# Optimization experiments

Measured on AMD Instinct MI355X. Metric: run time of the kernel, lower is better.

Reference implementation:

```python
import jax, jax.numpy as jnp
import numpy as np

N = 8192
D = 512
EPS = 1e-12  # F.normalize default eps


def setup_inputs() -> dict:
    key = jax.random.key(0)
    k1, k2 = jax.random.split(key)
    cur = jax.random.normal(k1, (N, D), dtype=jnp.float32)
    # randn -> mixed-sign entries, so every row of (incidence_m > 0) is unique
    # (the only case where the original `incidence_m += head` shapes agree).
    incidence_m = jax.random.normal(k2, (N, N), dtype=jnp.float32)
    return {"cur": cur, "incidence_m": incidence_m}


def reference(cur, incidence_m):
    # construct_directed: dedup rows of (incidence_m > 0); with all rows unique,
    # each node is its own hyperedge leader and head == mask as float, row order
    # preserved. head is built from python ints in torch, hence non-differentiable.
    mask = incidence_m > 0
    head = jax.lax.stop_gradient(mask.astype(incidence_m.dtype))  # [N, N]
    # F.normalize(head, dim=-1): L2 per row with eps clamp
    head = head / jnp.maximum(
        jnp.sqrt(jnp.sum(head * head, axis=-1, keepdims=True)), EPS
    )
    inc = incidence_m + head                          # [N, N]
    edge_fea = inc @ cur                              # [N, D]
    edge_degree = jnp.sum(inc, axis=-1, keepdims=True)  # [N, 1]
    return edge_fea / edge_degree
```

## Files before the change

### kernel.cpp

```cpp
#include <hip/hip_runtime.h>
#include <stdint.h>


#define NROWS 8192
#define DDIM  512

typedef float f32x4 __attribute__((ext_vector_type(4)));
typedef short s16x8 __attribute__((ext_vector_type(8)));

__device__ __forceinline__ unsigned short f2bf(float f) {
  union { float f; unsigned int u; } c; c.f = f;
  unsigned int u = c.u;
  unsigned int r = u + 0x7FFFu + ((u >> 16) & 1u);
  return (unsigned short)(r >> 16);
}

__global__ __launch_bounds__(256) void bprep_kernel(const float* __restrict__ cur,
                                                    unsigned char* __restrict__ bws) {
  int idx = blockIdx.x * 256 + threadIdx.x;
  int n = idx & 511;
  int kg9 = idx >> 9;
  int kt = kg9 >> 3;
  int kg = kg9 & 7;
  int k0 = kt * 64 + kg * 8;
  union { unsigned short h[8]; uint4 q; } u;
#pragma unroll
  for (int e = 0; e < 8; ++e)
    u.h[e] = f2bf(cur[(size_t)(k0 + e) * DDIM + n]);
  int nt = n >> 8, nn = n & 255;
  size_t off = ((size_t)(nt * 128 + kt) << 15) + ((size_t)kg << 12) + ((size_t)nn << 4);
  *(uint4*)(bws + off) = u.q;
}


#define FENCE() __builtin_amdgcn_sched_barrier(0)
#define BARRIER() __builtin_amdgcn_s_barrier()
#define WAITLGKM() asm volatile("s_waitcnt lgkmcnt(0)" ::: "memory")
#define MFMA_ __builtin_amdgcn_mfma_f32_16x16x32_bf16

__global__ __launch_bounds__(512, 4) void gemm_kernel(const float* __restrict__ inc,
                                                      const unsigned char* __restrict__ bws,
                                                      float* __restrict__ out) {
  __shared__ __align__(16) unsigned char smem[16512];
  unsigned char* const buf0 = smem;
  unsigned char* const buf1 = smem + 8192;

  const int tid = threadIdx.x;
  const int lane = tid & 63;
  const int wv = tid >> 6;
  const int r = lane & 15;
  const int q = lane >> 4;

  const int id = blockIdx.x;
  const int nt = (id & 7) >> 2;
  const int mt = (id >> 3) * 4 + (id & 3);
  const int brow = mt * 32;

  const int sm = tid >> 4;
  const int sp = tid & 15;
  const int kgw = sp >> 1, half = sp & 1;
  const float4* gAr = (const float4*)(inc + (size_t)(brow + sm) * NROWS) + sp;
  const int aWr = (kgw << 9) + ((sm ^ kgw) << 4) + (half << 3);

  int aOff[2][2];
#pragma unroll
  for (int kh = 0; kh < 2; ++kh)
#pragma unroll
    for (int rg = 0; rg < 2; ++rg) {
      int kg = kh * 4 + q;
      int row = rg * 16 + r;
      aOff[kh][rg] = (kg << 9) + ((row ^ kg) << 4);
    }

  const unsigned char* gB = bws + ((size_t)(nt * 128) << 15);
  int bOff[4];
#pragma unroll
  for (int kh = 0; kh < 2; ++kh)
#pragma unroll
    for (int cg = 0; cg < 2; ++cg)
      bOff[kh * 2 + cg] = ((kh * 4 + q) << 12) + ((wv * 32 + cg * 16 + r) << 4);

  f32x4 acc1[2][2], acc2[2][2];
#pragma unroll
  for (int a = 0; a < 2; ++a)
#pragma unroll
    for (int b = 0; b < 2; ++b) {
      acc1[a][b] = (f32x4){0.f, 0.f, 0.f, 0.f};
      acc2[a][b] = (f32x4){0.f, 0.f, 0.f, 0.f};
    }

  double s1 = 0.0;
  int cnt = 0;
  float4 x, y;
  s16x8 bX[4], bY[4];

#define ISSUE_A(d, KT) do { d = gAr[(KT) * 16]; } while (0)

#define LOADB(BS, KT) do {                                                                \
    const unsigned char* _g = gB + ((size_t)(KT) << 15);                                  \
    BS[0] = *(const s16x8*)(_g + bOff[0]);                                                \
    BS[1] = *(const s16x8*)(_g + bOff[1]);                                                \
    BS[2] = *(const s16x8*)(_g + bOff[2]);                                                \
    BS[3] = *(const s16x8*)(_g + bOff[3]);                                                \
  } while (0)

#define XFORM(v, BUF) do {                                                                \
    s1 += (double)v.x + (double)v.y + (double)v.z + (double)v.w;                          \
    cnt += (v.x > 0.f) + (v.y > 0.f) + (v.z > 0.f) + (v.w > 0.f);                         \
    unsigned dlo, dhi;                                                                    \
    asm("v_cvt_pk_bf16_f32 %0, %1, %2" : "=v"(dlo) : "v"(v.x), "v"(v.y));                 \
    asm("v_cvt_pk_bf16_f32 %0, %1, %2" : "=v"(dhi) : "v"(v.z), "v"(v.w));                 \
    unsigned mlo = (v.x > 0.f ? 0x3F80u : 0u) | (v.y > 0.f ? 0x3F800000u : 0u);           \
    unsigned mhi = (v.z > 0.f ? 0x3F80u : 0u) | (v.w > 0.f ? 0x3F800000u : 0u);           \
    *(unsigned long long*)((BUF) + aWr) =                                                 \
        (unsigned long long)dlo | ((unsigned long long)dhi << 32);                        \
    *(unsigned long long*)((BUF) + 4096 + aWr) =                                          \
        (unsigned long long)mlo | ((unsigned long long)mhi << 32);                        \
  } while (0)

#define MFMA_TILE(BUF, BS) do {                                                           \
    _Pragma("unroll")                                                                     \
    for (int kh = 0; kh < 2; ++kh) {                                                      \
      s16x8 af0 = *(const s16x8*)((BUF) + aOff[kh][0]);                                   \
      s16x8 af1 = *(const s16x8*)((BUF) + aOff[kh][1]);                                   \
      s16x8 mf0 = *(const s16x8*)((BUF) + 4096 + aOff[kh][0]);                            \
      s16x8 mf1 = *(const s16x8*)((BUF) + 4096 + aOff[kh][1]);                            \
      __builtin_amdgcn_s_setprio(1);                                                      \
      acc1[0][0] = MFMA_(af0, BS[kh * 2 + 0], acc1[0][0], 0, 0, 0);                       \
      acc2[0][0] = MFMA_(mf0, BS[kh * 2 + 0], acc2[0][0], 0, 0, 0);                       \
      acc1[0][1] = MFMA_(af0, BS[kh * 2 + 1], acc1[0][1], 0, 0, 0);                       \
      acc2[0][1] = MFMA_(mf0, BS[kh * 2 + 1], acc2[0][1], 0, 0, 0);                       \
      acc1[1][0] = MFMA_(af1, BS[kh * 2 + 0], acc1[1][0], 0, 0, 0);                       \
      acc2[1][0] = MFMA_(mf1, BS[kh * 2 + 0], acc2[1][0], 0, 0, 0);                       \
      acc1[1][1] = MFMA_(af1, BS[kh * 2 + 1], acc1[1][1], 0, 0, 0);                       \
      acc2[1][1] = MFMA_(mf1, BS[kh * 2 + 1], acc2[1][1], 0, 0, 0);                       \
      __builtin_amdgcn_s_setprio(0);                                                      \
    }                                                                                     \
  } while (0)

#define SYNC() do { FENCE(); WAITLGKM(); FENCE(); BARRIER(); FENCE(); } while (0)

  ISSUE_A(x, 0);
  LOADB(bX, 0);
  ISSUE_A(y, 1);
  XFORM(x, buf0);
  SYNC();

  for (int kt = 0; kt < 126; kt += 2) {
    ISSUE_A(x, kt + 2);
    LOADB(bY, kt + 1);
    FENCE();
    MFMA_TILE(buf0, bX);
    XFORM(y, buf1);
    SYNC();
    ISSUE_A(y, kt + 3);
    LOADB(bX, kt + 2);
    FENCE();
    MFMA_TILE(buf1, bY);
    XFORM(x, buf0);
    SYNC();
  }

  LOADB(bY, 127);
  FENCE();
  MFMA_TILE(buf0, bX);
  XFORM(y, buf1);
  SYNC();
  MFMA_TILE(buf1, bY);

#pragma unroll
  for (int o = 1; o < 16; o <<= 1) {
    s1 += __shfl_xor(s1, o);
    cnt += __shfl_xor(cnt, o);
  }
  __syncthreads();
  float* const invsS = (float*)buf0;
  float* const rdegS = invsS + 32;
  if (sp == 0) {
    double sq = sqrt((double)cnt);
    invsS[sm] = (cnt > 0) ? (float)(1.0 / sq) : 0.0f;
    rdegS[sm] = (float)(1.0 / (s1 + sq));
  }
  __syncthreads();

#pragma unroll
  for (int rg = 0; rg < 2; ++rg) {
#pragma unroll
    for (int cg = 0; cg < 2; ++cg) {
#pragma unroll
      for (int j = 0; j < 4; ++j) {
        int row = rg * 16 + q * 4 + j;
        out[(size_t)(brow + row) * DDIM + nt * 256 + wv * 32 + cg * 16 + r] =
            (acc1[rg][cg][j] + invsS[row] * acc2[rg][cg][j]) * rdegS[row];
      }
    }
  }
#undef ISSUE_A
#undef LOADB
#undef XFORM
#undef MFMA_TILE
#undef SYNC
}

extern "C" void kernel_launch(void* const* d_in, const int* in_sizes, int n_in,
                              void* d_out, int out_size, void* d_ws, size_t ws_size,
                              hipStream_t stream) {
  const float* cur = (const float*)d_in[0];
  const float* incm = (const float*)d_in[1];
  float* out = (float*)d_out;
  unsigned char* bws = (unsigned char*)d_ws;

  hipLaunchKernelGGL(bprep_kernel, dim3((NROWS * DDIM / 8) / 256), dim3(256), 0, stream,
                     cur, bws);
  hipLaunchKernelGGL(gemm_kernel, dim3(512), dim3(512), 0, stream, incm, bws, out);
}
```

Before: 166.9 us.

## Retile waves to 2x4 grid with half-tile B prefetch pipelining

```diff
diff --git a/kernel.cpp b/kernel.cpp
--- a/kernel.cpp
+++ b/kernel.cpp
@@ -48,6 +48,8 @@
   const int tid = threadIdx.x;
   const int lane = tid & 63;
   const int wv = tid >> 6;
+  const int wr = wv >> 2;
+  const int wc = wv & 3;
   const int r = lane & 15;
   const int q = lane >> 4;
 
@@ -62,46 +64,42 @@
   const float4* gAr = (const float4*)(inc + (size_t)(brow + sm) * NROWS) + sp;
   const int aWr = (kgw << 9) + ((sm ^ kgw) << 4) + (half << 3);
 
-  int aOff[2][2];
+  int aOff[2];
+#pragma unroll
+  for (int kh = 0; kh < 2; ++kh) {
+    int kg = kh * 4 + q;
+    int row = wr * 16 + r;
+    aOff[kh] = (kg << 9) + ((row ^ kg) << 4);
+  }
+
+  const unsigned char* gB = bws + ((size_t)(nt * 128) << 15);
+  int bOff[2][4];
 #pragma unroll
   for (int kh = 0; kh < 2; ++kh)
 #pragma unroll
-    for (int rg = 0; rg < 2; ++rg) {
-      int kg = kh * 4 + q;
-      int row = rg * 16 + r;
-      aOff[kh][rg] = (kg << 9) + ((row ^ kg) << 4);
-    }
-
-  const unsigned char* gB = bws + ((size_t)(nt * 128) << 15);
-  int bOff[4];
-#pragma unroll
-  for (int kh = 0; kh < 2; ++kh)
-#pragma unroll
-    for (int cg = 0; cg < 2; ++cg)
-      bOff[kh * 2 + cg] = ((kh * 4 + q) << 12) + ((wv * 32 + cg * 16 + r) << 4);
-
-  f32x4 acc1[2][2], acc2[2][2];
-#pragma unroll
-  for (int a = 0; a < 2; ++a)
-#pragma unroll
-    for (int b = 0; b < 2; ++b) {
-      acc1[a][b] = (f32x4){0.f, 0.f, 0.f, 0.f};
-      acc2[a][b] = (f32x4){0.f, 0.f, 0.f, 0.f};
-    }
+    for (int cg = 0; cg < 4; ++cg)
+      bOff[kh][cg] = ((kh * 4 + q) << 12) + ((wc * 64 + cg * 16 + r) << 4);
+
+  f32x4 acc1[4], acc2[4];
+#pragma unroll
+  for (int b = 0; b < 4; ++b) {
+    acc1[b] = (f32x4){0.f, 0.f, 0.f, 0.f};
+    acc2[b] = (f32x4){0.f, 0.f, 0.f, 0.f};
+  }
 
   double s1 = 0.0;
   int cnt = 0;
   float4 x, y;
-  s16x8 bX[4], bY[4];
+  s16x8 bA[4], bB[4];
 
 #define ISSUE_A(d, KT) do { d = gAr[(KT) * 16]; } while (0)
 
-#define LOADB(BS, KT) do {                                                                \
+#define LOADB(BS, KT, KH) do {                                                            \
     const unsigned char* _g = gB + ((size_t)(KT) << 15);                                  \
-    BS[0] = *(const s16x8*)(_g + bOff[0]);                                                \
-    BS[1] = *(const s16x8*)(_g + bOff[1]);                                                \
-    BS[2] = *(const s16x8*)(_g + bOff[2]);                                                \
-    BS[3] = *(const s16x8*)(_g + bOff[3]);                                                \
+    BS[0] = *(const s16x8*)(_g + bOff[KH][0]);                                            \
+    BS[1] = *(const s16x8*)(_g + bOff[KH][1]);                                            \
+    BS[2] = *(const s16x8*)(_g + bOff[KH][2]);                                            \
+    BS[3] = *(const s16x8*)(_g + bOff[KH][3]);                                            \
   } while (0)
 
 #define XFORM(v, BUF) do {                                                                \
@@ -118,55 +116,63 @@
         (unsigned long long)mlo | ((unsigned long long)mhi << 32);                        \
   } while (0)
 
-#define MFMA_TILE(BUF, BS) do {                                                           \
-    _Pragma("unroll")                                                                     \
-    for (int kh = 0; kh < 2; ++kh) {                                                      \
-      s16x8 af0 = *(const s16x8*)((BUF) + aOff[kh][0]);                                   \
-      s16x8 af1 = *(const s16x8*)((BUF) + aOff[kh][1]);                                   \
-      s16x8 mf0 = *(const s16x8*)((BUF) + 4096 + aOff[kh][0]);                            \
-      s16x8 mf1 = *(const s16x8*)((BUF) + 4096 + aOff[kh][1]);                            \
-      __builtin_amdgcn_s_setprio(1);                                                      \
-      acc1[0][0] = MFMA_(af0, BS[kh * 2 + 0], acc1[0][0], 0, 0, 0);                       \
-      acc2[0][0] = MFMA_(mf0, BS[kh * 2 + 0], acc2[0][0], 0, 0, 0);                       \
-      acc1[0][1] = MFMA_(af0, BS[kh * 2 + 1], acc1[0][1], 0, 0, 0);                       \
-      acc2[0][1] = MFMA_(mf0, BS[kh * 2 + 1], acc2[0][1], 0, 0, 0);                       \
-      acc1[1][0] = MFMA_(af1, BS[kh * 2 + 0], acc1[1][0], 0, 0, 0);                       \
-      acc2[1][0] = MFMA_(mf1, BS[kh * 2 + 0], acc2[1][0], 0, 0, 0);                       \
-      acc1[1][1] = MFMA_(af1, BS[kh * 2 + 1], acc1[1][1], 0, 0, 0);                       \
-      acc2[1][1] = MFMA_(mf1, BS[kh * 2 + 1], acc2[1][1], 0, 0, 0);                       \
-      __builtin_amdgcn_s_setprio(0);                                                      \
-    }                                                                                     \
+#define MFMA_KH(BUF, KH, BS) do {                                                         \
+    s16x8 af = *(const s16x8*)((BUF) + aOff[KH]);                                         \
+    s16x8 mf = *(const s16x8*)((BUF) + 4096 + aOff[KH]);                                  \
+    __builtin_amdgcn_s_setprio(1);                                                        \
+    acc1[0] = MFMA_(af, BS[0], acc1[0], 0, 0, 0);                                         \
+    acc2[0] = MFMA_(mf, BS[0], acc2[0], 0, 0, 0);                                         \
+    acc1[1] = MFMA_(af, BS[1], acc1[1], 0, 0, 0);                                         \
+    acc2[1] = MFMA_(mf, BS[1], acc2[1], 0, 0, 0);                                         \
+    acc1[2] = MFMA_(af, BS[2], acc1[2], 0, 0, 0);                                         \
+    acc2[2] = MFMA_(mf, BS[2], acc2[2], 0, 0, 0);                                         \
+    acc1[3] = MFMA_(af, BS[3], acc1[3], 0, 0, 0);                                         \
+    acc2[3] = MFMA_(mf, BS[3], acc2[3], 0, 0, 0);                                         \
+    __builtin_amdgcn_s_setprio(0);                                                        \
   } while (0)
 
 #define SYNC() do { FENCE(); WAITLGKM(); FENCE(); BARRIER(); FENCE(); } while (0)
 
   ISSUE_A(x, 0);
-  LOADB(bX, 0);
+  LOADB(bA, 0, 0);
   ISSUE_A(y, 1);
   XFORM(x, buf0);
   SYNC();
 
   for (int kt = 0; kt < 126; kt += 2) {
     ISSUE_A(x, kt + 2);
-    LOADB(bY, kt + 1);
-    FENCE();
-    MFMA_TILE(buf0, bX);
+    LOADB(bB, kt, 1);
+    FENCE();
+    MFMA_KH(buf0, 0, bA);
+    LOADB(bA, kt + 1, 0);
+    FENCE();
+    MFMA_KH(buf0, 1, bB);
     XFORM(y, buf1);
     SYNC();
     ISSUE_A(y, kt + 3);
-    LOADB(bX, kt + 2);
-    FENCE();
-    MFMA_TILE(buf1, bY);
+    LOADB(bB, kt + 1, 1);
+    FENCE();
+    MFMA_KH(buf1, 0, bA);
+    LOADB(bA, kt + 2, 0);
+    FENCE();
+    MFMA_KH(buf1, 1, bB);
     XFORM(x, buf0);
     SYNC();
   }
 
-  LOADB(bY, 127);
-  FENCE();
-  MFMA_TILE(buf0, bX);
+  LOADB(bB, 126, 1);
+  FENCE();
+  MFMA_KH(buf0, 0, bA);
+  LOADB(bA, 127, 0);
+  FENCE();
+  MFMA_KH(buf0, 1, bB);
   XFORM(y, buf1);
   SYNC();
-  MFMA_TILE(buf1, bY);
+  LOADB(bB, 127, 1);
+  FENCE();
+  MFMA_KH(buf1, 0, bA);
+  FENCE();
+  MFMA_KH(buf1, 1, bB);
 
 #pragma unroll
   for (int o = 1; o < 16; o <<= 1) {
@@ -184,21 +190,18 @@
   __syncthreads();
 
 #pragma unroll
-  for (int rg = 0; rg < 2; ++rg) {
-#pragma unroll
-    for (int cg = 0; cg < 2; ++cg) {
-#pragma unroll
-      for (int j = 0; j < 4; ++j) {
-        int row = rg * 16 + q * 4 + j;
-        out[(size_t)(brow + row) * DDIM + nt * 256 + wv * 32 + cg * 16 + r] =
-            (acc1[rg][cg][j] + invsS[row] * acc2[rg][cg][j]) * rdegS[row];
-      }
+  for (int cg = 0; cg < 4; ++cg) {
+#pragma unroll
+    for (int j = 0; j < 4; ++j) {
+      int row = wr * 16 + q * 4 + j;
+      out[(size_t)(brow + row) * DDIM + nt * 256 + wc * 64 + cg * 16 + r] =
+          (acc1[cg][j] + invsS[row] * acc2[cg][j]) * rdegS[row];
     }
   }
 #undef ISSUE_A
 #undef LOADB
 #undef XFORM
-#undef MFMA_TILE
+#undef MFMA_KH
 #undef SYNC
 }
 
```

New measurement: 232.3 us. 39.1% more time.

## Deepen A-tile pipeline to four LDS buffers with two barriers per four k-tiles

Applied to the files above, without the earlier changes.

```diff
diff --git a/kernel.cpp b/kernel.cpp
--- a/kernel.cpp
+++ b/kernel.cpp
@@ -41,9 +41,11 @@
 __global__ __launch_bounds__(512, 4) void gemm_kernel(const float* __restrict__ inc,
                                                       const unsigned char* __restrict__ bws,
                                                       float* __restrict__ out) {
-  __shared__ __align__(16) unsigned char smem[16512];
+  __shared__ __align__(16) unsigned char smem[32768];
   unsigned char* const buf0 = smem;
   unsigned char* const buf1 = smem + 8192;
+  unsigned char* const buf2 = smem + 16384;
+  unsigned char* const buf3 = smem + 24576;
 
   const int tid = threadIdx.x;
   const int lane = tid & 63;
@@ -91,7 +93,7 @@
 
   double s1 = 0.0;
   int cnt = 0;
-  float4 x, y;
+  float4 x0, y0, x1, y1;
   s16x8 bX[4], bY[4];
 
 #define ISSUE_A(d, KT) do { d = gAr[(KT) * 16]; } while (0)
@@ -140,33 +142,55 @@
 
 #define SYNC() do { FENCE(); WAITLGKM(); FENCE(); BARRIER(); FENCE(); } while (0)
 
-  ISSUE_A(x, 0);
+  ISSUE_A(x0, 0);
   LOADB(bX, 0);
-  ISSUE_A(y, 1);
-  XFORM(x, buf0);
+  ISSUE_A(y0, 1);
+  ISSUE_A(x1, 2);
+  ISSUE_A(y1, 3);
+  XFORM(x0, buf0);
+  XFORM(y0, buf1);
   SYNC();
 
-  for (int kt = 0; kt < 126; kt += 2) {
-    ISSUE_A(x, kt + 2);
-    LOADB(bY, kt + 1);
+  for (int i = 0; i < 31; ++i) {
+    const int t = i * 4;
+    ISSUE_A(x0, t + 4);
+    ISSUE_A(y0, t + 5);
+    LOADB(bY, t + 1);
     FENCE();
     MFMA_TILE(buf0, bX);
-    XFORM(y, buf1);
+    XFORM(x1, buf2);
+    LOADB(bX, t + 2);
+    FENCE();
+    MFMA_TILE(buf1, bY);
+    XFORM(y1, buf3);
     SYNC();
-    ISSUE_A(y, kt + 3);
-    LOADB(bX, kt + 2);
-    FENCE();
-    MFMA_TILE(buf1, bY);
-    XFORM(x, buf0);
+    ISSUE_A(x1, t + 6);
+    ISSUE_A(y1, t + 7);
+    LOADB(bY, t + 3);
+    FENCE();
+    MFMA_TILE(buf2, bX);
+    XFORM(x0, buf0);
+    LOADB(bX, t + 4);
+    FENCE();
+    MFMA_TILE(buf3, bY);
+    XFORM(y0, buf1);
     SYNC();
   }
 
+  LOADB(bY, 125);
+  FENCE();
+  MFMA_TILE(buf0, bX);
+  XFORM(x1, buf2);
+  LOADB(bX, 126);
+  FENCE();
+  MFMA_TILE(buf1, bY);
+  XFORM(y1, buf3);
+  SYNC();
   LOADB(bY, 127);
   FENCE();
-  MFMA_TILE(buf0, bX);
-  XFORM(y, buf1);
-  SYNC();
-  MFMA_TILE(buf1, bY);
+  MFMA_TILE(buf2, bX);
+  FENCE();
+  MFMA_TILE(buf3, bY);
 
 #pragma unroll
   for (int o = 1; o < 16; o <<= 1) {
```

New measurement: 176.1 us. 5.5% more time.

## Split waves into value and mask roles with wider column tiles, reduce via LDS

Applied to the files above, without the earlier changes.

```diff
diff --git a/kernel.cpp b/kernel.cpp
--- a/kernel.cpp
+++ b/kernel.cpp
@@ -41,13 +41,18 @@
 __global__ __launch_bounds__(512, 4) void gemm_kernel(const float* __restrict__ inc,
                                                       const unsigned char* __restrict__ bws,
                                                       float* __restrict__ out) {
-  __shared__ __align__(16) unsigned char smem[16512];
+  __shared__ __align__(16) unsigned char smem[33024];
   unsigned char* const buf0 = smem;
   unsigned char* const buf1 = smem + 8192;
+  float* const invsS = (float*)(smem + 32768);
+  float* const rdegS = invsS + 32;
 
   const int tid = threadIdx.x;
   const int lane = tid & 63;
   const int wv = tid >> 6;
+  const int wc = wv & 3;
+  const int role = wv >> 2;
+  const int roleOff = role << 12;
   const int r = lane & 15;
   const int q = lane >> 4;
 
@@ -73,26 +78,24 @@
     }
 
   const unsigned char* gB = bws + ((size_t)(nt * 128) << 15);
-  int bOff[4];
+  int bOff[8];
 #pragma unroll
   for (int kh = 0; kh < 2; ++kh)
 #pragma unroll
-    for (int cg = 0; cg < 2; ++cg)
-      bOff[kh * 2 + cg] = ((kh * 4 + q) << 12) + ((wv * 32 + cg * 16 + r) << 4);
-
-  f32x4 acc1[2][2], acc2[2][2];
+    for (int cg = 0; cg < 4; ++cg)
+      bOff[kh * 4 + cg] = ((kh * 4 + q) << 12) + ((wc * 64 + cg * 16 + r) << 4);
+
+  f32x4 acc[2][4];
 #pragma unroll
   for (int a = 0; a < 2; ++a)
 #pragma unroll
-    for (int b = 0; b < 2; ++b) {
-      acc1[a][b] = (f32x4){0.f, 0.f, 0.f, 0.f};
-      acc2[a][b] = (f32x4){0.f, 0.f, 0.f, 0.f};
-    }
+    for (int b = 0; b < 4; ++b)
+      acc[a][b] = (f32x4){0.f, 0.f, 0.f, 0.f};
 
   double s1 = 0.0;
   int cnt = 0;
   float4 x, y;
-  s16x8 bX[4], bY[4];
+  s16x8 bX[8], bY[8];
 
 #define ISSUE_A(d, KT) do { d = gAr[(KT) * 16]; } while (0)
 
@@ -102,6 +105,10 @@
     BS[1] = *(const s16x8*)(_g + bOff[1]);                                                \
     BS[2] = *(const s16x8*)(_g + bOff[2]);                                                \
     BS[3] = *(const s16x8*)(_g + bOff[3]);                                                \
+    BS[4] = *(const s16x8*)(_g + bOff[4]);                                                \
+    BS[5] = *(const s16x8*)(_g + bOff[5]);                                                \
+    BS[6] = *(const s16x8*)(_g + bOff[6]);                                                \
+    BS[7] = *(const s16x8*)(_g + bOff[7]);                                                \
   } while (0)
 
 #define XFORM(v, BUF) do {                                                                \
@@ -121,19 +128,17 @@
 #define MFMA_TILE(BUF, BS) do {                                                           \
     _Pragma("unroll")                                                                     \
     for (int kh = 0; kh < 2; ++kh) {                                                      \
-      s16x8 af0 = *(const s16x8*)((BUF) + aOff[kh][0]);                                   \
-      s16x8 af1 = *(const s16x8*)((BUF) + aOff[kh][1]);                                   \
-      s16x8 mf0 = *(const s16x8*)((BUF) + 4096 + aOff[kh][0]);                            \
-      s16x8 mf1 = *(const s16x8*)((BUF) + 4096 + aOff[kh][1]);                            \
+      s16x8 f0 = *(const s16x8*)((BUF) + roleOff + aOff[kh][0]);                          \
+      s16x8 f1 = *(const s16x8*)((BUF) + roleOff + aOff[kh][1]);                          \
       __builtin_amdgcn_s_setprio(1);                                                      \
-      acc1[0][0] = MFMA_(af0, BS[kh * 2 + 0], acc1[0][0], 0, 0, 0);                       \
-      acc2[0][0] = MFMA_(mf0, BS[kh * 2 + 0], acc2[0][0], 0, 0, 0);                       \
-      acc1[0][1] = MFMA_(af0, BS[kh * 2 + 1], acc1[0][1], 0, 0, 0);                       \
-      acc2[0][1] = MFMA_(mf0, BS[kh * 2 + 1], acc2[0][1], 0, 0, 0);                       \
-      acc1[1][0] = MFMA_(af1, BS[kh * 2 + 0], acc1[1][0], 0, 0, 0);                       \
-      acc2[1][0] = MFMA_(mf1, BS[kh * 2 + 0], acc2[1][0], 0, 0, 0);                       \
-      acc1[1][1] = MFMA_(af1, BS[kh * 2 + 1], acc1[1][1], 0, 0, 0);                       \
-      acc2[1][1] = MFMA_(mf1, BS[kh * 2 + 1], acc2[1][1], 0, 0, 0);                       \
+      acc[0][0] = MFMA_(f0, BS[kh * 4 + 0], acc[0][0], 0, 0, 0);                          \
+      acc[0][1] = MFMA_(f0, BS[kh * 4 + 1], acc[0][1], 0, 0, 0);                          \
+      acc[0][2] = MFMA_(f0, BS[kh * 4 + 2], acc[0][2], 0, 0, 0);                          \
+      acc[0][3] = MFMA_(f0, BS[kh * 4 + 3], acc[0][3], 0, 0, 0);                          \
+      acc[1][0] = MFMA_(f1, BS[kh * 4 + 0], acc[1][0], 0, 0, 0);                          \
+      acc[1][1] = MFMA_(f1, BS[kh * 4 + 1], acc[1][1], 0, 0, 0);                          \
+      acc[1][2] = MFMA_(f1, BS[kh * 4 + 2], acc[1][2], 0, 0, 0);                          \
+      acc[1][3] = MFMA_(f1, BS[kh * 4 + 3], acc[1][3], 0, 0, 0);                          \
       __builtin_amdgcn_s_setprio(0);                                                      \
     }                                                                                     \
   } while (0)
@@ -174,8 +179,6 @@
     cnt += __shfl_xor(cnt, o);
   }
   __syncthreads();
-  float* const invsS = (float*)buf0;
-  float* const rdegS = invsS + 32;
   if (sp == 0) {
     double sq = sqrt((double)cnt);
     invsS[sm] = (cnt > 0) ? (float)(1.0 / sq) : 0.0f;
@@ -183,17 +186,31 @@
   }
   __syncthreads();
 
-#pragma unroll
-  for (int rg = 0; rg < 2; ++rg) {
-#pragma unroll
-    for (int cg = 0; cg < 2; ++cg) {
-#pragma unroll
-      for (int j = 0; j < 4; ++j) {
-        int row = rg * 16 + q * 4 + j;
-        out[(size_t)(brow + row) * DDIM + nt * 256 + wv * 32 + cg * 16 + r] =
-            (acc1[rg][cg][j] + invsS[row] * acc2[rg][cg][j]) * rdegS[row];
-      }
-    }
+  float* const eBuf = (float*)smem;
+  if (role == 1) {
+#pragma unroll
+    for (int rg = 0; rg < 2; ++rg)
+#pragma unroll
+      for (int cg = 0; cg < 4; ++cg)
+#pragma unroll
+        for (int j = 0; j < 4; ++j) {
+          int row = rg * 16 + q * 4 + j;
+          eBuf[row * 256 + wc * 64 + cg * 16 + r] = acc[rg][cg][j] * invsS[row];
+        }
+  }
+  __syncthreads();
+  if (role == 0) {
+#pragma unroll
+    for (int rg = 0; rg < 2; ++rg)
+#pragma unroll
+      for (int cg = 0; cg < 4; ++cg)
+#pragma unroll
+        for (int j = 0; j < 4; ++j) {
+          int row = rg * 16 + q * 4 + j;
+          int col = wc * 64 + cg * 16 + r;
+          out[(size_t)(brow + row) * DDIM + nt * 256 + col] =
+              (acc[rg][cg][j] + eBuf[row * 256 + col]) * rdegS[row];
+        }
   }
 #undef ISSUE_A
 #undef LOADB
```

After: 416.8 us. +149.7%, slower.
